# Optimization experiments

Hardware: AMD Instinct MI355X
Metric: run time of the kernel (lower is better)

The kernel has to match this reference:

```python
import jax, jax.numpy as jnp
import numpy as np

B, T, P, D = 8, 2048, 4, 768

def setup_inputs() -> dict:
    key = jax.random.key(0)
    k1, k2, k3 = jax.random.split(key, 3)
    text_inputs = jax.random.normal(k1, (B, T, D), dtype=jnp.float32)
    sit_mask = jax.random.randint(k2, (B, T), 0, 2).astype(jnp.float32)
    proposition_matrix = jax.random.normal(k3, (B, T, P, D), dtype=jnp.float32)
    return {"text_inputs": text_inputs, "sit_mask": sit_mask, "proposition_matrix": proposition_matrix}

def reference(text_inputs, sit_mask, proposition_matrix):
    # D from proposition_matrix (matches text hidden dim), used for softmax scaling
    d = proposition_matrix.shape[-1]
    t = text_inputs.shape[1]
    # raw scores [B,T,T], scaled by 1/sqrt(D)
    scores = jnp.einsum('bid,bjd->bij', text_inputs, text_inputs) * (1.0 / jnp.sqrt(jnp.asarray(d, text_inputs.dtype)))
    # causal mask: strictly upper triangular -> -inf (tokens attend to self + past)
    causal = jnp.tril(jnp.ones((t, t), dtype=bool))  # [T,T]
    scores = jnp.where(causal[None, :, :], scores, -jnp.inf)
    weights = jax.nn.softmax(scores, axis=2)
    # padding mask via outer product of sit_mask; zero AFTER softmax (no renorm), as in original
    pad = (sit_mask[:, :, None] * sit_mask[:, None, :]) != 0  # [B,T,T]
    weights = jnp.where(pad, weights, jnp.zeros((), weights.dtype))
    out = jnp.einsum('bij,bjd->bid', weights, text_inputs)  # [B,T,D]
    # concat_self_hidden=True
    out = jnp.concatenate([out, text_inputs], axis=-1)  # [B,T,2D]
    return out
```

## Files before the change

kernel.cpp:

```cpp
#include <hip/hip_runtime.h>
#include <math.h>

constexpr int kT = 2048;
constexpr int kD = 768;

typedef __attribute__((ext_vector_type(8))) short short8;
typedef __attribute__((ext_vector_type(4))) float f32x4;
typedef __attribute__((ext_vector_type(16))) float f32x16;

#define FB(f) __builtin_bit_cast(unsigned, (f))
__device__ __forceinline__ unsigned pk_hi16(unsigned hi, unsigned lo) {
  return __builtin_amdgcn_perm(hi, lo, 0x07060302);
}
__device__ __forceinline__ unsigned pk_lo16(unsigned hi, unsigned lo) {
  return __builtin_amdgcn_perm(hi, lo, 0x05040100);
}

__global__ __launch_bounds__(256, 2) void attn_mfma2(
    const float* __restrict__ x, const float* __restrict__ mask,
    float* __restrict__ out)
{
  const int tid = threadIdx.x;
  const int w = tid >> 6, l = tid & 63;
  const int l15 = l & 15, q4 = l >> 4;
  const int l31 = l & 31, h2 = l >> 5;

  const int bid = (int)blockIdx.x;
  const int qt = (bid < 256) ? (2 * bid) : (511 - 2 * (bid - 256));
  const int b = qt >> 6;
  const int i0 = (qt & 63) << 5;

  const float* xb = x + (size_t)b * kT * kD;
  const float* mrow = mask + (size_t)b * kT;

  __shared__ unsigned short xK[16][776];
  __shared__ unsigned short VTb[192 * 64];
  __shared__ float sPart[4][16][36];
  __shared__ unsigned short Pm[32][16];
  __shared__ float corrS[32];
  __shared__ float invlS[32];

  short8 qf[2][6];
#pragma unroll
  for (int mt = 0; mt < 2; ++mt) {
    const int row = i0 + 16 * mt + l15;
#pragma unroll
    for (int s = 0; s < 6; ++s) {
      const float* p = xb + (size_t)row * kD + 192 * w + 32 * s + 8 * q4;
      float4 f0 = *(const float4*)p;
      float4 f1 = *(const float4*)(p + 4);
      uint4 u;
      u.x = pk_hi16(FB(f0.y), FB(f0.x));
      u.y = pk_hi16(FB(f0.w), FB(f0.z));
      u.z = pk_hi16(FB(f1.y), FB(f1.x));
      u.w = pk_hi16(FB(f1.w), FB(f1.z));
      qf[mt][s] = __builtin_bit_cast(short8, u);
    }
  }

  f32x16 o[6];
#pragma unroll
  for (int nt = 0; nt < 6; ++nt)
#pragma unroll
    for (int e = 0; e < 16; ++e) o[nt][e] = 0.0f;

  float mrun = -INFINITY, lrun = 0.0f;
  const float scale = 0.036084391824351615f;
  const int nTiles = i0 / 16 + 2;

  const int q = tid & 7, sr = tid >> 3;
  const int jA = (q >> 1) + 8 * (q & 1);
  const int irow = i0 + sr;

  const int D0 = 48 * w + (l31 >> 2);
  const int vtb_off0 = D0 * 64 + (((l31 & 3) ^ (D0 & 3)) << 4)
                     + ((8 * h2) ^ (8 * ((l31 >> 4) & 1)));

  float4 pf[3][4];
#pragma unroll
  for (int it = 0; it < 3; ++it)
#pragma unroll
    for (int jj = 0; jj < 4; ++jj)
      pf[it][jj] = *(const float4*)(xb + (size_t)(q4 + 4 * jj) * kD
                                    + 4 * (l15 + 16 * it + 48 * w));

  for (int t = 0; t < nTiles; ++t) {
    const int j0 = t * 16;
    __syncthreads();

#pragma unroll
    for (int it = 0; it < 3; ++it) {
      const int d4 = l15 + 16 * it + 48 * w;
      unsigned lo[4], hi[4];
#pragma unroll
      for (int jj = 0; jj < 4; ++jj) {
        lo[jj] = pk_hi16(FB(pf[it][jj].y), FB(pf[it][jj].x));
        hi[jj] = pk_hi16(FB(pf[it][jj].w), FB(pf[it][jj].z));
      }
#pragma unroll
      for (int jj = 0; jj < 4; ++jj) {
        uint2 v; v.x = lo[jj]; v.y = hi[jj];
        *(uint2*)&xK[q4 + 4 * jj][4 * d4] = v;
      }
      const int D = d4;
      const int jb = (4 * q4) ^ (8 * ((D >> 2) & 1));
      const int base = D * 64 + jb;
      uint2 v;
      v.x = pk_lo16(lo[1], lo[0]); v.y = pk_lo16(lo[3], lo[2]);
      *(uint2*)&VTb[base + (((0 ^ (D & 3))) << 4)] = v;
      v.x = pk_hi16(lo[1], lo[0]); v.y = pk_hi16(lo[3], lo[2]);
      *(uint2*)&VTb[base + (((1 ^ (D & 3))) << 4)] = v;
      v.x = pk_lo16(hi[1], hi[0]); v.y = pk_lo16(hi[3], hi[2]);
      *(uint2*)&VTb[base + (((2 ^ (D & 3))) << 4)] = v;
      v.x = pk_hi16(hi[1], hi[0]); v.y = pk_hi16(hi[3], hi[2]);
      *(uint2*)&VTb[base + (((3 ^ (D & 3))) << 4)] = v;
    }

    if (t + 1 < nTiles) {
      const int jn = j0 + 16;
#pragma unroll
      for (int it = 0; it < 3; ++it)
#pragma unroll
        for (int jj = 0; jj < 4; ++jj)
          pf[it][jj] = *(const float4*)(xb + (size_t)(jn + q4 + 4 * jj) * kD
                                        + 4 * (l15 + 16 * it + 48 * w));
    }
    __syncthreads();

    {
      f32x4 sf0, sf1;
#pragma unroll
      for (int e = 0; e < 4; ++e) { sf0[e] = 0.f; sf1[e] = 0.f; }
#pragma unroll
      for (int s = 0; s < 6; ++s) {
        short8 kb = *(const short8*)&xK[l15][192 * w + 32 * s + 8 * q4];
        sf0 = __builtin_amdgcn_mfma_f32_16x16x32_bf16(qf[0][s], kb, sf0, 0, 0, 0);
        sf1 = __builtin_amdgcn_mfma_f32_16x16x32_bf16(qf[1][s], kb, sf1, 0, 0, 0);
      }
      *(f32x4*)&sPart[w][l15][4 * q4]      = sf0;
      *(f32x4*)&sPart[w][l15][16 + 4 * q4] = sf1;
    }
    __syncthreads();

    {
      float s0 = 0.f, s1 = 0.f;
#pragma unroll
      for (int ww = 0; ww < 4; ++ww) {
        s0 += sPart[ww][jA][sr];
        s1 += sPart[ww][jA + 4][sr];
      }
      const int ja = j0 + jA, jb_ = j0 + jA + 4;
      float a0 = (ja  <= irow) ? s0 * scale : -INFINITY;
      float a1 = (jb_ <= irow) ? s1 * scale : -INFINITY;
      float loc = fmaxf(a0, a1);
      loc = fmaxf(loc, __shfl_xor(loc, 1, 64));
      loc = fmaxf(loc, __shfl_xor(loc, 2, 64));
      loc = fmaxf(loc, __shfl_xor(loc, 4, 64));
      const float mn = fmaxf(mrun, loc);
      const float corr = __expf(mrun - mn);
      const float p0 = __expf(a0 - mn);
      const float p1 = __expf(a1 - mn);
      float rs = p0 + p1;
      rs += __shfl_xor(rs, 1, 64);
      rs += __shfl_xor(rs, 2, 64);
      rs += __shfl_xor(rs, 4, 64);
      lrun = lrun * corr + rs;
      mrun = mn;
      const float w0 = (mrow[ja]  != 0.f) ? p0 : 0.f;
      const float w1 = (mrow[jb_] != 0.f) ? p1 : 0.f;
      *(unsigned*)&Pm[sr][2 * q] = pk_hi16(FB(w1), FB(w0));
      if (q == 0) corrS[sr] = corr;
    }
    __syncthreads();

    {
      float cr[16];
      bool need = false;
#pragma unroll
      for (int e4 = 0; e4 < 4; ++e4) {
        f32x4 qd = *(const f32x4*)&corrS[8 * e4 + 4 * h2];
#pragma unroll
        for (int ee = 0; ee < 4; ++ee) {
          cr[4 * e4 + ee] = qd[ee];
          need |= (qd[ee] != 1.0f);
        }
      }
      if (__any(need)) {
#pragma unroll
        for (int nt = 0; nt < 6; ++nt)
#pragma unroll
          for (int e = 0; e < 16; ++e) o[nt][e] *= cr[e];
      }
      short8 pa = *(const short8*)&Pm[l31][8 * h2];
#pragma unroll
      for (int nt = 0; nt < 6; ++nt) {
        short8 vb = *(const short8*)&VTb[vtb_off0 + 512 * nt];
        o[nt] = __builtin_amdgcn_mfma_f32_32x32x16_bf16(pa, vb, o[nt], 0, 0, 0);
      }
    }
  }

  if (q == 0) invlS[sr] = (mrow[irow] != 0.f) ? 1.0f / lrun : 0.0f;
  __syncthreads();
  {
    float il[16];
#pragma unroll
    for (int e4 = 0; e4 < 4; ++e4) {
      f32x4 qd = *(const f32x4*)&invlS[8 * e4 + 4 * h2];
#pragma unroll
      for (int ee = 0; ee < 4; ++ee) il[4 * e4 + ee] = qd[ee];
    }
    float* ob = out + (size_t)(b * kT + i0) * (2 * kD);
#pragma unroll
    for (int nt = 0; nt < 6; ++nt) {
      const int col = 192 * w + 32 * nt + l31;
#pragma unroll
      for (int e = 0; e < 16; ++e) {
        const int row = (e & 3) + 8 * (e >> 2) + 4 * h2;
        ob[(size_t)row * (2 * kD) + col] = o[nt][e] * il[e];
      }
    }
#pragma unroll
    for (int pass = 0; pass < 2; ++pass) {
      const int rr = (tid >> 4) + 16 * pass;
      const float* srcr = xb + (size_t)(i0 + rr) * kD;
      float* dstr = ob + (size_t)rr * (2 * kD) + kD;
#pragma unroll
      for (int it = 0; it < 12; ++it) {
        const int d4 = (tid & 15) + 16 * it;
        *(float4*)(dstr + 4 * d4) = *(const float4*)(srcr + 4 * d4);
      }
    }
  }
}

extern "C" void kernel_launch(void* const* d_in, const int* in_sizes, int n_in,
                              void* d_out, int out_size, void* d_ws, size_t ws_size,
                              hipStream_t stream) {
  const float* x    = (const float*)d_in[0];
  const float* mask = (const float*)d_in[1];
  float* out = (float*)d_out;
  attn_mfma2<<<dim3(512), dim3(256), 0, stream>>>(x, mask, out);
}
```

Measured before the change: 500.5 us.

## Use LDS-only barriers, hoist mask loads, reorder block schedule, drop rescale branch

Replaces __syncthreads with a barrier that waits only on LDS counters (lgkmcnt), so the global prefetch loads of the next tile stay in flight across barriers. Mask values are loaded at the top of each tile iteration instead of inside the softmax section. Block-to-tile mapping changes to interleave batches with longest query tiles first. The conditional skip of the output rescale becomes an unconditional multiply. The custom waitcnt encoding carries risk if it does not correctly cover the prefetch registers consumed later.

After: 487.5 us. -2.6%, faster.

```diff
diff --git a/kernel.cpp b/kernel.cpp
--- a/kernel.cpp
+++ b/kernel.cpp
@@ -16,7 +16,14 @@
   return __builtin_amdgcn_perm(hi, lo, 0x05040100);
 }
 
-__global__ __launch_bounds__(256, 2) void attn_mfma2(
+__device__ __forceinline__ void lds_barrier() {
+  asm volatile("" ::: "memory");
+  __builtin_amdgcn_s_waitcnt(0xC07F);
+  __builtin_amdgcn_s_barrier();
+  asm volatile("" ::: "memory");
+}
+
+__global__ __launch_bounds__(256, 2) void attn_mfma3(
     const float* __restrict__ x, const float* __restrict__ mask,
     float* __restrict__ out)
 {
@@ -26,9 +33,8 @@
   const int l31 = l & 31, h2 = l >> 5;
 
   const int bid = (int)blockIdx.x;
-  const int qt = (bid < 256) ? (2 * bid) : (511 - 2 * (bid - 256));
-  const int b = qt >> 6;
-  const int i0 = (qt & 63) << 5;
+  const int b  = bid & 7;
+  const int i0 = (63 - (bid >> 3)) << 5;
 
   const float* xb = x + (size_t)b * kT * kD;
   const float* mrow = mask + (size_t)b * kT;
@@ -86,7 +92,10 @@
 
   for (int t = 0; t < nTiles; ++t) {
     const int j0 = t * 16;
-    __syncthreads();
+    const float mskA = mrow[j0 + jA];
+    const float mskB = mrow[j0 + jA + 4];
+
+    lds_barrier();
 
 #pragma unroll
     for (int it = 0; it < 3; ++it) {
@@ -125,7 +134,7 @@
           pf[it][jj] = *(const float4*)(xb + (size_t)(jn + q4 + 4 * jj) * kD
                                         + 4 * (l15 + 16 * it + 48 * w));
     }
-    __syncthreads();
+    lds_barrier();
 
     {
       f32x4 sf0, sf1;
@@ -140,7 +149,7 @@
       *(f32x4*)&sPart[w][l15][4 * q4]      = sf0;
       *(f32x4*)&sPart[w][l15][16 + 4 * q4] = sf1;
     }
-    __syncthreads();
+    lds_barrier();
 
     {
       float s0 = 0.f, s1 = 0.f;
@@ -166,31 +175,25 @@
       rs += __shfl_xor(rs, 4, 64);
       lrun = lrun * corr + rs;
       mrun = mn;
-      const float w0 = (mrow[ja]  != 0.f) ? p0 : 0.f;
-      const float w1 = (mrow[jb_] != 0.f) ? p1 : 0.f;
+      const float w0 = (mskA != 0.f) ? p0 : 0.f;
+      const float w1 = (mskB != 0.f) ? p1 : 0.f;
       *(unsigned*)&Pm[sr][2 * q] = pk_hi16(FB(w1), FB(w0));
       if (q == 0) corrS[sr] = corr;
     }
-    __syncthreads();
+    lds_barrier();
 
     {
       float cr[16];
-      bool need = false;
 #pragma unroll
       for (int e4 = 0; e4 < 4; ++e4) {
         f32x4 qd = *(const f32x4*)&corrS[8 * e4 + 4 * h2];
 #pragma unroll
-        for (int ee = 0; ee < 4; ++ee) {
-          cr[4 * e4 + ee] = qd[ee];
-          need |= (qd[ee] != 1.0f);
-        }
-      }
-      if (__any(need)) {
-#pragma unroll
-        for (int nt = 0; nt < 6; ++nt)
-#pragma unroll
-          for (int e = 0; e < 16; ++e) o[nt][e] *= cr[e];
-      }
+        for (int ee = 0; ee < 4; ++ee) cr[4 * e4 + ee] = qd[ee];
+      }
+#pragma unroll
+      for (int nt = 0; nt < 6; ++nt)
+#pragma unroll
+        for (int e = 0; e < 16; ++e) o[nt][e] *= cr[e];
       short8 pa = *(const short8*)&Pm[l31][8 * h2];
 #pragma unroll
       for (int nt = 0; nt < 6; ++nt) {
@@ -201,7 +204,7 @@
   }
 
   if (q == 0) invlS[sr] = (mrow[irow] != 0.f) ? 1.0f / lrun : 0.0f;
-  __syncthreads();
+  lds_barrier();
   {
     float il[16];
 #pragma unroll
@@ -240,5 +243,5 @@
   const float* x    = (const float*)d_in[0];
   const float* mask = (const float*)d_in[1];
   float* out = (float*)d_out;
-  attn_mfma2<<<dim3(512), dim3(256), 0, stream>>>(x, mask, out);
-}
+  attn_mfma3<<<dim3(512), dim3(256), 0, stream>>>(x, mask, out);
+}
```
